# Optimization experiments

Measured on AMD Instinct MI355X. Metric: run time of the kernel, lower is better.

The kernel has to match this reference:

```python
import jax, jax.numpy as jnp
import numpy as np

MASK_INFTY_APPROX = 1e30
B, L, D = 2, 2048, 1024
H = 16
HD = D // H  # 64
NCODE = 512


def setup_inputs() -> dict:
    key = jax.random.key(0)
    ks = jax.random.split(key, 6)
    s = 1.0 / np.sqrt(D)
    x = jax.random.normal(ks[0], (B, L, D), dtype=jnp.float32)
    Wq = jax.random.normal(ks[1], (D, D), dtype=jnp.float32) * s
    Wk = jax.random.normal(ks[2], (D, D), dtype=jnp.float32) * s
    Wv = jax.random.normal(ks[3], (D, D), dtype=jnp.float32) * s
    Wo = jax.random.normal(ks[4], (D, D), dtype=jnp.float32) * s
    codebook = jax.random.normal(ks[5], (H, NCODE, HD), dtype=jnp.float32)
    return {"x": x, "Wq": Wq, "Wk": Wk, "Wv": Wv, "Wo": Wo, "codebook": codebook}


def _vq(k, codebook):
    # k: [B,H,L,hd], codebook: [H,C,hd]
    dot = jnp.einsum('bhld,hcd->bhlc', k, codebook)
    k2 = jnp.sum(k * k, axis=-1, keepdims=True)            # [B,H,L,1]
    c2 = jnp.sum(codebook * codebook, axis=-1)             # [H,C]
    d2 = k2 - 2.0 * dot + c2[None, :, None, :]             # [B,H,L,C]
    shortcodes = jnp.argmin(d2, axis=-1)                   # [B,H,L]
    h_idx = jnp.arange(H)[None, :, None]
    c_sel = codebook[h_idx, shortcodes]                    # [B,H,L,hd]
    # straight-through quantization
    k_hat = k + jax.lax.stop_gradient(c_sel - k)
    l_commit = jnp.mean(jnp.sum((k - jax.lax.stop_gradient(c_sel)) ** 2, axis=-1))
    l_codebook = jnp.mean(jnp.sum((jax.lax.stop_gradient(k) - c_sel) ** 2, axis=-1))
    return k_hat, shortcodes, l_commit, l_codebook


def reference(x, Wq, Wk, Wv, Wo, codebook):
    q = jnp.einsum('bld,de->ble', x, Wq.T).reshape(B, L, H, HD).transpose(0, 2, 1, 3)
    k = jnp.einsum('bld,de->ble', x, Wk.T).reshape(B, L, H, HD).transpose(0, 2, 1, 3)
    v = jnp.einsum('bld,de->ble', x, Wv.T).reshape(B, L, H, HD).transpose(0, 2, 1, 3)
    k_hat, shortcodes, l_commit, l_codebook = _vq(k, codebook)
    scale = HD ** (-0.5)
    logits = jnp.einsum('bhld,bhtd->bhlt', q, k_hat) * scale  # [B,H,L,L]
    causal_mask = jnp.tril(jnp.ones((L, L), dtype=bool))
    logits = jnp.where(causal_mask[None, None], logits, -MASK_INFTY_APPROX)
    w = jax.nn.softmax(logits, axis=-1)
    attn = jnp.einsum('bhlt,bhtd->bhld', w, v)
    attn = attn.transpose(0, 2, 1, 3).reshape(B, L, D)
    out = jnp.einsum('bld,de->ble', attn, Wo.T)
    return out, l_commit, l_codebook, shortcodes
```

## Files before the change

### kernel.cpp

```cpp
#include <hip/hip_runtime.h>
#include <stdint.h>

#define BB 2
#define HH 16
#define LL 2048
#define DD 1024
#define HDD 64
#define NC 512

typedef __bf16 bf16x8 __attribute__((ext_vector_type(8)));
typedef float f32x4 __attribute__((ext_vector_type(4)));
typedef unsigned short u16x8 __attribute__((ext_vector_type(8)));

__device__ __forceinline__ unsigned short f2bf(float f) {
  union { float f; unsigned u; } v; v.f = f;
  unsigned u = v.u;
  u += 0x7fffu + ((u >> 16) & 1u);
  return (unsigned short)(u >> 16);
}
__device__ __forceinline__ float bf2f(unsigned short h) {
  union { unsigned u; float f; } v; v.u = ((unsigned)h) << 16;
  return v.f;
}

__device__ __forceinline__ void load_lds16(const unsigned short* g, unsigned short* l) {
  __builtin_amdgcn_global_load_lds((const __attribute__((address_space(1))) void*)g,
                                   (__attribute__((address_space(3))) void*)l, 16, 0, 0);
}

__global__ void cast_all(const float* __restrict__ x, const float* __restrict__ wq,
                         const float* __restrict__ wk, const float* __restrict__ wv,
                         const float* __restrict__ wo, const float* __restrict__ cb,
                         unsigned short* __restrict__ xb, unsigned short* __restrict__ xl,
                         unsigned short* __restrict__ wb, unsigned short* __restrict__ wkl,
                         unsigned short* __restrict__ wob, unsigned short* __restrict__ cbb,
                         unsigned short* __restrict__ cbl, float* __restrict__ lsum) {
  long i = (long)blockIdx.x * blockDim.x + threadIdx.x;
  if (i == 0) lsum[0] = 0.f;
  const long NX = 4194304, NW = 1048576, NCB = 524288;
  const long TOT = NX + 4 * NW + NCB;
  for (long t = i; t < TOT; t += (long)gridDim.x * blockDim.x) {
    if (t < NX) {
      float v = x[t];
      unsigned short hi = f2bf(v);
      xb[t] = hi;
      xl[t] = f2bf(v - bf2f(hi));
    } else if (t < NX + NW) {
      wb[t - NX] = f2bf(wq[t - NX]);
    } else if (t < NX + 2 * NW) {
      long idx = t - NX - NW;
      float v = wk[idx];
      unsigned short hi = f2bf(v);
      wb[NW + idx] = hi;
      wkl[idx] = f2bf(v - bf2f(hi));
    } else if (t < NX + 3 * NW) {
      wb[t - NX] = f2bf(wv[t - NX - 2 * NW]);
    } else if (t < NX + 4 * NW) {
      wob[t - NX - 3 * NW] = f2bf(wo[t - NX - 3 * NW]);
    } else {
      long idx = t - NX - 4 * NW;
      float v = cb[idx];
      unsigned short hi = f2bf(v);
      cbb[idx] = hi;
      cbl[idx] = f2bf(v - bf2f(hi));
    }
  }
}

__global__ void c2_kernel(const float* __restrict__ cb, float* __restrict__ c2) {
  int i = blockIdx.x * blockDim.x + threadIdx.x;
  if (i >= HH * NC) return;
  const float* r = cb + (long)i * HDD;
  double s = 0.0;
  for (int j = 0; j < HDD; j++) s += (double)r[j] * (double)r[j];
  c2[i] = (float)s;
}

__global__ __launch_bounds__(256) void gemm_qv(
    const unsigned short* __restrict__ xb, const unsigned short* __restrict__ wb,
    unsigned short* __restrict__ qb, unsigned short* __restrict__ vt) {
  __shared__ __align__(16) unsigned short As[128 * 32];
  __shared__ __align__(16) unsigned short Bs[128 * 32];
  int tid = threadIdx.x;
  int wave = tid >> 6, lane = tid & 63;
  int quad = lane >> 4, col = lane & 15;
  int m0 = blockIdx.y * 128;
  int n0 = blockIdx.x * 128 + (blockIdx.x >= 8 ? 1024 : 0);
  f32x4 acc[4][4] = {};
  int row_in = (wave << 4) + (lane >> 2);
  int seg = lane & 3;
  const unsigned short* gA0 = xb + (long)(m0 + row_in) * DD + seg * 8;
  const unsigned short* gA1 = xb + (long)(m0 + 64 + row_in) * DD + seg * 8;
  const unsigned short* gB0 = wb + (long)(n0 + row_in) * DD + seg * 8;
  const unsigned short* gB1 = wb + (long)(n0 + 64 + row_in) * DD + seg * 8;
  unsigned short* lA0 = As + wave * 512;
  unsigned short* lA1 = As + 2048 + wave * 512;
  unsigned short* lB0 = Bs + wave * 512;
  unsigned short* lB1 = Bs + 2048 + wave * 512;
  int wm = wave & 1, wn = wave >> 1;
  const unsigned short* pa = As + (wm * 64 + col) * 32 + quad * 8;
  const unsigned short* pb = Bs + (wn * 64 + col) * 32 + quad * 8;
  for (int kk = 0; kk < DD; kk += 32) {
    __syncthreads();
    load_lds16(gA0 + kk, lA0);
    load_lds16(gA1 + kk, lA1);
    load_lds16(gB0 + kk, lB0);
    load_lds16(gB1 + kk, lB1);
    __syncthreads();
    bf16x8 af[4], bfr[4];
    for (int t = 0; t < 4; t++) af[t]  = *(const bf16x8*)(pa + t * 512);
    for (int t = 0; t < 4; t++) bfr[t] = *(const bf16x8*)(pb + t * 512);
    for (int mt = 0; mt < 4; mt++)
      for (int nt = 0; nt < 4; nt++)
        acc[mt][nt] = __builtin_amdgcn_mfma_f32_16x16x32_bf16(af[mt], bfr[nt], acc[mt][nt], 0, 0, 0);
  }
  for (int mt = 0; mt < 4; mt++)
    for (int nt = 0; nt < 4; nt++) {
      int mbase = m0 + wm * 64 + mt * 16 + quad * 4;
      int n = n0 + wn * 64 + nt * 16 + col;
      int which = n >> 10, e = n & 1023;
      int h = e >> 6, hd = e & 63;
      for (int r = 0; r < 4; r++) {
        int m = mbase + r;
        int b = m >> 11, l = m & 2047;
        unsigned short val = f2bf(acc[mt][nt][r]);
        long bh = (long)(b * HH + h);
        if (which == 0)      qb[(bh * LL + l) * HDD + hd] = val;
        else                 vt[(bh * HDD + hd) * LL + l] = val;
      }
    }
}

__global__ __launch_bounds__(256) void kgemm_split(
    const unsigned short* __restrict__ xb, const unsigned short* __restrict__ xl,
    const unsigned short* __restrict__ wb, const unsigned short* __restrict__ wkl,
    float* __restrict__ kf) {
  __shared__ __align__(16) unsigned short Ah[128 * 32];
  __shared__ __align__(16) unsigned short Al[128 * 32];
  __shared__ __align__(16) unsigned short Bh[64 * 32];
  __shared__ __align__(16) unsigned short Bl[64 * 32];
  int tid = threadIdx.x;
  int wave = tid >> 6, lane = tid & 63;
  int quad = lane >> 4, col = lane & 15;
  int n0 = blockIdx.x * 64;
  int m0 = blockIdx.y * 128;
  f32x4 acc[4][2] = {};
  int row_in = (wave << 4) + (lane >> 2);
  int seg = lane & 3;
  const unsigned short* gAh0 = xb + (long)(m0 + row_in) * DD + seg * 8;
  const unsigned short* gAh1 = xb + (long)(m0 + 64 + row_in) * DD + seg * 8;
  const unsigned short* gAl0 = xl + (long)(m0 + row_in) * DD + seg * 8;
  const unsigned short* gAl1 = xl + (long)(m0 + 64 + row_in) * DD + seg * 8;
  const unsigned short* gBh  = wb + (long)(1048576 + (long)(n0 + row_in) * DD) + seg * 8;
  const unsigned short* gBl  = wkl + (long)(n0 + row_in) * DD + seg * 8;
  unsigned short* lAh0 = Ah + wave * 512;
  unsigned short* lAh1 = Ah + 2048 + wave * 512;
  unsigned short* lAl0 = Al + wave * 512;
  unsigned short* lAl1 = Al + 2048 + wave * 512;
  unsigned short* lBh  = Bh + wave * 512;
  unsigned short* lBl  = Bl + wave * 512;
  int wm = wave & 1, wn = wave >> 1;
  const unsigned short* pah = Ah + (wm * 64 + col) * 32 + quad * 8;
  const unsigned short* pal = Al + (wm * 64 + col) * 32 + quad * 8;
  const unsigned short* pbh = Bh + (wn * 32 + col) * 32 + quad * 8;
  const unsigned short* pbl = Bl + (wn * 32 + col) * 32 + quad * 8;
  for (int kk = 0; kk < DD; kk += 32) {
    __syncthreads();
    load_lds16(gAh0 + kk, lAh0);
    load_lds16(gAh1 + kk, lAh1);
    load_lds16(gAl0 + kk, lAl0);
    load_lds16(gAl1 + kk, lAl1);
    load_lds16(gBh + kk, lBh);
    load_lds16(gBl + kk, lBl);
    __syncthreads();
    bf16x8 ah[4], al[4], bhf[2], blf[2];
    for (int t = 0; t < 4; t++) ah[t] = *(const bf16x8*)(pah + t * 512);
    for (int t = 0; t < 4; t++) al[t] = *(const bf16x8*)(pal + t * 512);
    for (int t = 0; t < 2; t++) bhf[t] = *(const bf16x8*)(pbh + t * 512);
    for (int t = 0; t < 2; t++) blf[t] = *(const bf16x8*)(pbl + t * 512);
    for (int mt = 0; mt < 4; mt++)
      for (int nt = 0; nt < 2; nt++) {
        acc[mt][nt] = __builtin_amdgcn_mfma_f32_16x16x32_bf16(ah[mt], bhf[nt], acc[mt][nt], 0, 0, 0);
        acc[mt][nt] = __builtin_amdgcn_mfma_f32_16x16x32_bf16(ah[mt], blf[nt], acc[mt][nt], 0, 0, 0);
        acc[mt][nt] = __builtin_amdgcn_mfma_f32_16x16x32_bf16(al[mt], bhf[nt], acc[mt][nt], 0, 0, 0);
      }
  }
  int h = blockIdx.x;
  for (int mt = 0; mt < 4; mt++)
    for (int nt = 0; nt < 2; nt++) {
      int mbase = m0 + wm * 64 + mt * 16 + quad * 4;
      int hd = wn * 32 + nt * 16 + col;
      for (int r = 0; r < 4; r++) {
        int m = mbase + r;
        int b = m >> 11, l = m & 2047;
        kf[((long)(b * HH + h) * LL + l) * HDD + hd] = acc[mt][nt][r];
      }
    }
}

__global__ __launch_bounds__(256) void vq_mfma(
    const float* __restrict__ kf, const float* __restrict__ cb,
    const float* __restrict__ c2, const unsigned short* __restrict__ cbb,
    const unsigned short* __restrict__ cbl,
    unsigned short* __restrict__ khat, float* __restrict__ scodes,
    float* __restrict__ lsum) {
  __shared__ __align__(16) unsigned short CbH[2][32 * 72];
  __shared__ __align__(16) unsigned short CbL[2][32 * 72];
  __shared__ int finalIdx[64];
  int tid = threadIdx.x, wave = tid >> 6, lane = tid & 63;
  int quad = lane >> 4, col = lane & 15;
  int rb = blockIdx.x;
  int bh = blockIdx.y;
  int h = bh & 15;
  int rbase = rb * 64 + wave * 16;
  const float* kp = kf + ((long)bh * LL + rbase + col) * HDD + quad * 8;
  float fv[16];
  {
    float4 t0 = *(const float4*)(kp);
    float4 t1 = *(const float4*)(kp + 4);
    float4 t2 = *(const float4*)(kp + 32);
    float4 t3 = *(const float4*)(kp + 36);
    fv[0]=t0.x; fv[1]=t0.y; fv[2]=t0.z; fv[3]=t0.w;
    fv[4]=t1.x; fv[5]=t1.y; fv[6]=t1.z; fv[7]=t1.w;
    fv[8]=t2.x; fv[9]=t2.y; fv[10]=t2.z; fv[11]=t2.w;
    fv[12]=t3.x; fv[13]=t3.y; fv[14]=t3.z; fv[15]=t3.w;
  }
  float k2 = 0.f;
#pragma unroll
  for (int j = 0; j < 16; j++) k2 = fmaf(fv[j], fv[j], k2);
  k2 += __shfl_xor(k2, 16);
  k2 += __shfl_xor(k2, 32);
  u16x8 kh0u, kh1u, kl0u, kl1u;
#pragma unroll
  for (int j = 0; j < 8; j++) {
    unsigned short hi = f2bf(fv[j]);
    kh0u[j] = hi; kl0u[j] = f2bf(fv[j] - bf2f(hi));
    unsigned short hi2 = f2bf(fv[8 + j]);
    kh1u[j] = hi2; kl1u[j] = f2bf(fv[8 + j] - bf2f(hi2));
  }
  bf16x8 bh0 = __builtin_bit_cast(bf16x8, kh0u);
  bf16x8 bh1 = __builtin_bit_cast(bf16x8, kh1u);
  bf16x8 bl0 = __builtin_bit_cast(bf16x8, kl0u);
  bf16x8 bl1 = __builtin_bit_cast(bf16x8, kl1u);
  const unsigned short* cbbh = cbb + (long)h * NC * HDD;
  const unsigned short* cblh = cbl + (long)h * NC * HDD;
  const float* c2h = c2 + h * NC;

  int srow = tid >> 3;
  int sseg = (tid & 7) * 8;
  const unsigned short* gH = cbbh + (long)srow * HDD + sseg;
  const unsigned short* gL = cblh + (long)srow * HDD + sseg;
  int ldsOff = srow * 72 + sseg;

  {
    u16x8 ph = *(const u16x8*)(gH);
    u16x8 pl = *(const u16x8*)(gL);
    *(u16x8*)(CbH[0] + ldsOff) = ph;
    *(u16x8*)(CbL[0] + ldsOff) = pl;
  }
  __syncthreads();

  float b1v = 1e38f, b2v = 1e38f;
  int b1i = 0x7fffffff, b2i = 0x7fffffff;
  for (int t = 0; t < 16; t++) {
    int cur = t & 1;
    u16x8 nh, nl;
    if (t < 15) {
      nh = *(const u16x8*)(gH + (t + 1) * 32 * HDD);
      nl = *(const u16x8*)(gL + (t + 1) * 32 * HDD);
    }
#pragma unroll
    for (int s = 0; s < 2; s++) {
      const unsigned short* rp = CbH[cur] + (s * 16 + col) * 72 + quad * 8;
      const unsigned short* rq = CbL[cur] + (s * 16 + col) * 72 + quad * 8;
      bf16x8 ah0 = *(const bf16x8*)(rp);
      bf16x8 ah1 = *(const bf16x8*)(rp + 32);
      bf16x8 al0 = *(const bf16x8*)(rq);
      bf16x8 al1 = *(const bf16x8*)(rq + 32);
      f32x4 aP = {}, aQ = {};
      aP = __builtin_amdgcn_mfma_f32_16x16x32_bf16(ah0, bh0, aP, 0, 0, 0);
      aQ = __builtin_amdgcn_mfma_f32_16x16x32_bf16(ah1, bh1, aQ, 0, 0, 0);
      aP = __builtin_amdgcn_mfma_f32_16x16x32_bf16(al0, bh0, aP, 0, 0, 0);
      aQ = __builtin_amdgcn_mfma_f32_16x16x32_bf16(al1, bh1, aQ, 0, 0, 0);
      aP = __builtin_amdgcn_mfma_f32_16x16x32_bf16(ah0, bl0, aP, 0, 0, 0);
      aQ = __builtin_amdgcn_mfma_f32_16x16x32_bf16(ah1, bl1, aQ, 0, 0, 0);
      f32x4 c2v = *(const f32x4*)(c2h + t * 32 + s * 16 + quad * 4);
#pragma unroll
      for (int r = 0; r < 4; r++) {
        float val = c2v[r] - 2.0f * (aP[r] + aQ[r]);
        int idx = t * 32 + s * 16 + quad * 4 + r;
        if (val < b1v) { b2v = b1v; b2i = b1i; b1v = val; b1i = idx; }
        else if (val < b2v) { b2v = val; b2i = idx; }
      }
    }
    if (t < 15) {
      *(u16x8*)(CbH[cur ^ 1] + ldsOff) = nh;
      *(u16x8*)(CbL[cur ^ 1] + ldsOff) = nl;
    }
    __syncthreads();
  }
#pragma unroll
  for (int d = 16; d <= 32; d <<= 1) {
    float o1v = __shfl_xor(b1v, d); int o1i = __shfl_xor(b1i, d);
    float o2v = __shfl_xor(b2v, d); int o2i = __shfl_xor(b2i, d);
    if (o1v < b1v || (o1v == b1v && o1i < b1i)) {
      float nv; int ni;
      if (b1v < o2v || (b1v == o2v && b1i < o2i)) { nv = b1v; ni = b1i; }
      else { nv = o2v; ni = o2i; }
      b1v = o1v; b1i = o1i; b2v = nv; b2i = ni;
    } else {
      if (o1v < b2v || (o1v == b2v && o1i < b2i)) { b2v = o1v; b2i = o1i; }
    }
  }
  const float DMARG = 0.015625f;
  bool trig = (b2v - b1v <= DMARG);
  float part;
  int widx = b1i;
  if (__any(trig)) {
    const float* kpr = kf + ((long)bh * LL + rbase + col) * HDD + quad * 8;
    float4 f0 = *(const float4*)(kpr);
    float4 f1 = *(const float4*)(kpr + 4);
    float4 f2 = *(const float4*)(kpr + 32);
    float4 f3 = *(const float4*)(kpr + 36);
    const float* c1p = cb + ((long)h * NC + b1i) * HDD + quad * 8;
    const float* c2p = cb + ((long)h * NC + b2i) * HDD + quad * 8;
    float4 a0 = *(const float4*)(c1p);
    float4 a1 = *(const float4*)(c1p + 4);
    float4 a2 = *(const float4*)(c1p + 32);
    float4 a3 = *(const float4*)(c1p + 36);
    float4 e0 = *(const float4*)(c2p);
    float4 e1 = *(const float4*)(c2p + 4);
    float4 e2 = *(const float4*)(c2p + 32);
    float4 e3 = *(const float4*)(c2p + 36);
    float s1 = 0.f, s2 = 0.f;
#pragma unroll
    for (int j = 0; j < 4; j++) {
      float d;
      d = ((const float*)&f0)[j] - ((const float*)&a0)[j]; s1 = fmaf(d, d, s1);
      d = ((const float*)&f1)[j] - ((const float*)&a1)[j]; s1 = fmaf(d, d, s1);
      d = ((const float*)&f2)[j] - ((const float*)&a2)[j]; s1 = fmaf(d, d, s1);
      d = ((const float*)&f3)[j] - ((const float*)&a3)[j]; s1 = fmaf(d, d, s1);
      d = ((const float*)&f0)[j] - ((const float*)&e0)[j]; s2 = fmaf(d, d, s2);
      d = ((const float*)&f1)[j] - ((const float*)&e1)[j]; s2 = fmaf(d, d, s2);
      d = ((const float*)&f2)[j] - ((const float*)&e2)[j]; s2 = fmaf(d, d, s2);
      d = ((const float*)&f3)[j] - ((const float*)&e3)[j]; s2 = fmaf(d, d, s2);
    }
    s1 += __shfl_xor(s1, 16); s1 += __shfl_xor(s1, 32);
    s2 += __shfl_xor(s2, 16); s2 += __shfl_xor(s2, 32);
    if (trig) {
      if (s2 < s1 || (s2 == s1 && b2i < b1i)) { widx = b2i; part = s2; }
      else { widx = b1i; part = s1; }
    } else {
      part = k2 + b1v;
    }
  } else {
    part = k2 + b1v;
  }
  if (quad != 0) part = 0.f;
  part += __shfl_xor(part, 1);  part += __shfl_xor(part, 2);
  part += __shfl_xor(part, 4);  part += __shfl_xor(part, 8);
  part += __shfl_xor(part, 16); part += __shfl_xor(part, 32);
  if (lane == 0) atomicAdd(lsum, part);
  if (lane < 16) {
    scodes[(long)bh * LL + rbase + lane] = (float)widx;
    finalIdx[wave * 16 + lane] = widx;
  }
  __syncthreads();
  {
    int r = tid >> 2, p = (tid & 3) * 16;
    int code = finalIdx[r];
    const unsigned short* src = cbb + ((long)h * NC + code) * HDD + p;
    unsigned short* dst = khat + ((long)bh * LL + rb * 64 + r) * HDD + p;
    *(u16x8*)(dst)     = *(const u16x8*)(src);
    *(u16x8*)(dst + 8) = *(const u16x8*)(src + 8);
  }
}

__global__ __launch_bounds__(256) void attn_kernel(
    const unsigned short* __restrict__ qb, const unsigned short* __restrict__ khat,
    const unsigned short* __restrict__ vt, unsigned short* __restrict__ attnb) {
  __shared__ __align__(16) unsigned short Pbuf[4][2][16 * 72];
  __shared__ __align__(16) unsigned short Kbuf[64 * 72];
  __shared__ __align__(16) unsigned short Vbuf[64 * 72];
  int tid = threadIdx.x, wave = tid >> 6, lane = tid & 63;
  int quad = lane >> 4, col = lane & 15;
  int pi = blockIdx.x;
  int bh = blockIdx.y;
  int b = bh >> 4, h = bh & 15;
  int ta = pi, tb = 31 - pi;
  int qbA = ta * 64 + wave * 16;
  int qbB = tb * 64 + wave * 16;
  const unsigned short* qrA = qb + ((long)bh * LL + qbA + col) * HDD;
  const unsigned short* qrB = qb + ((long)bh * LL + qbB + col) * HDD;
  bf16x8 aqA0 = *(const bf16x8*)(qrA + quad * 8);
  bf16x8 aqA1 = *(const bf16x8*)(qrA + 32 + quad * 8);
  bf16x8 aqB0 = *(const bf16x8*)(qrB + quad * 8);
  bf16x8 aqB1 = *(const bf16x8*)(qrB + 32 + quad * 8);
  float lA[4] = {0.f, 0.f, 0.f, 0.f}, lB[4] = {0.f, 0.f, 0.f, 0.f};
  f32x4 oA[4] = {}, oB[4] = {};
  unsigned short* PA = Pbuf[wave][0];
  unsigned short* PB = Pbuf[wave][1];
  const unsigned short* kh = khat + (long)bh * LL * HDD;
  const unsigned short* vh = vt + (long)bh * HDD * LL;
  int srow = tid >> 2, sc = (tid & 3) * 8;
  const unsigned short* gK = kh + (long)srow * HDD + sc;
  const unsigned short* gV = vh + (long)srow * LL + sc;
  unsigned short* lK = Kbuf + srow * 72 + sc;
  unsigned short* lV = Vbuf + srow * 72 + sc;
  const float SCL = 0.18033688011112042f;
  for (int kt = 0; kt <= tb; kt++) {
    int kbase = kt * 64;
    bool actA = (kt <= ta);
    __syncthreads();
    {
      const unsigned short* srcK = gK + (long)kbase * HDD;
      const unsigned short* srcV = gV + kbase;
      *(u16x8*)lK        = *(const u16x8*)(srcK);
      *(u16x8*)(lK + 32) = *(const u16x8*)(srcK + 32);
      *(u16x8*)lV        = *(const u16x8*)(srcV);
      *(u16x8*)(lV + 32) = *(const u16x8*)(srcV + 32);
    }
    __syncthreads();
    f32x4 zA[4], zB[4];
    for (int nt = 0; nt < 4; nt++) {
      const unsigned short* krow = Kbuf + (nt * 16 + col) * 72;
      bf16x8 k0 = *(const bf16x8*)(krow + quad * 8);
      bf16x8 k1 = *(const bf16x8*)(krow + 32 + quad * 8);
      f32x4 z = {};
      z = __builtin_amdgcn_mfma_f32_16x16x32_bf16(aqB0, k0, z, 0, 0, 0);
      z = __builtin_amdgcn_mfma_f32_16x16x32_bf16(aqB1, k1, z, 0, 0, 0);
      zB[nt] = z;
      if (actA) {
        f32x4 y = {};
        y = __builtin_amdgcn_mfma_f32_16x16x32_bf16(aqA0, k0, y, 0, 0, 0);
        y = __builtin_amdgcn_mfma_f32_16x16x32_bf16(aqA1, k1, y, 0, 0, 0);
        zA[nt] = y;
      }
    }
    for (int nt = 0; nt < 4; nt++) {
      int key = kbase + nt * 16 + col;
      for (int r = 0; r < 4; r++) {
        float sc2 = zB[nt][r] * SCL;
        if (kt == tb && key > qbB + quad * 4 + r) sc2 = -1e30f;
        float p = exp2f(sc2);
        lB[r] += p;
        PB[(quad * 4 + r) * 72 + nt * 16 + col] = __builtin_bit_cast(unsigned short, (__bf16)p);
      }
    }
    if (actA) {
      for (int nt = 0; nt < 4; nt++) {
        int key = kbase + nt * 16 + col;
        for (int r = 0; r < 4; r++) {
          float sc2 = zA[nt][r] * SCL;
          if (kt == ta && key > qbA + quad * 4 + r) sc2 = -1e30f;
          float p = exp2f(sc2);
          lA[r] += p;
          PA[(quad * 4 + r) * 72 + nt * 16 + col] = __builtin_bit_cast(unsigned short, (__bf16)p);
        }
      }
    }
    bf16x8 apB0 = *(const bf16x8*)(PB + col * 72 + quad * 8);
    bf16x8 apB1 = *(const bf16x8*)(PB + col * 72 + 32 + quad * 8);
    bf16x8 apA0, apA1;
    if (actA) {
      apA0 = *(const bf16x8*)(PA + col * 72 + quad * 8);
      apA1 = *(const bf16x8*)(PA + col * 72 + 32 + quad * 8);
    }
    for (int nt = 0; nt < 4; nt++) {
      const unsigned short* vrow = Vbuf + (nt * 16 + col) * 72;
      bf16x8 v0 = *(const bf16x8*)(vrow + quad * 8);
      bf16x8 v1 = *(const bf16x8*)(vrow + 32 + quad * 8);
      oB[nt] = __builtin_amdgcn_mfma_f32_16x16x32_bf16(apB0, v0, oB[nt], 0, 0, 0);
      oB[nt] = __builtin_amdgcn_mfma_f32_16x16x32_bf16(apB1, v1, oB[nt], 0, 0, 0);
      if (actA) {
        oA[nt] = __builtin_amdgcn_mfma_f32_16x16x32_bf16(apA0, v0, oA[nt], 0, 0, 0);
        oA[nt] = __builtin_amdgcn_mfma_f32_16x16x32_bf16(apA1, v1, oA[nt], 0, 0, 0);
      }
    }
  }
  float invA[4], invB[4];
  for (int r = 0; r < 4; r++) {
    float t = lA[r];
    t += __shfl_xor(t, 1); t += __shfl_xor(t, 2);
    t += __shfl_xor(t, 4); t += __shfl_xor(t, 8);
    invA[r] = 1.0f / t;
    float u = lB[r];
    u += __shfl_xor(u, 1); u += __shfl_xor(u, 2);
    u += __shfl_xor(u, 4); u += __shfl_xor(u, 8);
    invB[r] = 1.0f / u;
  }
  for (int r = 0; r < 4; r++) {
    int rowA = qbA + quad * 4 + r;
    int rowB = qbB + quad * 4 + r;
    for (int nt = 0; nt < 4; nt++) {
      int hd = nt * 16 + col;
      attnb[((long)b * LL + rowA) * DD + h * HDD + hd] = f2bf(oA[nt][r] * invA[r]);
      attnb[((long)b * LL + rowB) * DD + h * HDD + hd] = f2bf(oB[nt][r] * invB[r]);
    }
  }
}

__global__ __launch_bounds__(256) void gemm_out(
    const unsigned short* __restrict__ attnb, const unsigned short* __restrict__ wob,
    float* __restrict__ out) {
  __shared__ __align__(16) unsigned short As[128 * 32];
  __shared__ __align__(16) unsigned short Bs[128 * 32];
  int tid = threadIdx.x;
  int wave = tid >> 6, lane = tid & 63;
  int quad = lane >> 4, col = lane & 15;
  int m0 = blockIdx.y * 128;
  int n0 = blockIdx.x * 128;
  f32x4 acc[4][4] = {};
  int row_in = (wave << 4) + (lane >> 2);
  int seg = lane & 3;
  const unsigned short* gA0 = attnb + (long)(m0 + row_in) * DD + seg * 8;
  const unsigned short* gA1 = attnb + (long)(m0 + 64 + row_in) * DD + seg * 8;
  const unsigned short* gB0 = wob + (long)(n0 + row_in) * DD + seg * 8;
  const unsigned short* gB1 = wob + (long)(n0 + 64 + row_in) * DD + seg * 8;
  unsigned short* lA0 = As + wave * 512;
  unsigned short* lA1 = As + 2048 + wave * 512;
  unsigned short* lB0 = Bs + wave * 512;
  unsigned short* lB1 = Bs + 2048 + wave * 512;
  int wm = wave & 1, wn = wave >> 1;
  const unsigned short* pa = As + (wm * 64 + col) * 32 + quad * 8;
  const unsigned short* pb = Bs + (wn * 64 + col) * 32 + quad * 8;
  for (int kk = 0; kk < DD; kk += 32) {
    __syncthreads();
    load_lds16(gA0 + kk, lA0);
    load_lds16(gA1 + kk, lA1);
    load_lds16(gB0 + kk, lB0);
    load_lds16(gB1 + kk, lB1);
    __syncthreads();
    bf16x8 af[4], bfr[4];
    for (int t = 0; t < 4; t++) af[t]  = *(const bf16x8*)(pa + t * 512);
    for (int t = 0; t < 4; t++) bfr[t] = *(const bf16x8*)(pb + t * 512);
    for (int mt = 0; mt < 4; mt++)
      for (int nt = 0; nt < 4; nt++)
        acc[mt][nt] = __builtin_amdgcn_mfma_f32_16x16x32_bf16(af[mt], bfr[nt], acc[mt][nt], 0, 0, 0);
  }
  for (int mt = 0; mt < 4; mt++)
    for (int nt = 0; nt < 4; nt++) {
      int mbase = m0 + wm * 64 + mt * 16 + quad * 4;
      int n = n0 + wn * 64 + nt * 16 + col;
      for (int r = 0; r < 4; r++)
        out[(long)(mbase + r) * DD + n] = acc[mt][nt][r];
    }
}

__global__ void finalize(const float* __restrict__ lsum, float* __restrict__ out) {
  if (threadIdx.x == 0) {
    float v = lsum[0] / (float)(BB * HH * LL);
    out[4194304] = v;
    out[4194305] = v;
  }
}

extern "C" void kernel_launch(void* const* d_in, const int* in_sizes, int n_in,
                              void* d_out, int out_size, void* d_ws, size_t ws_size,
                              hipStream_t stream) {
  const float* x  = (const float*)d_in[0];
  const float* wq = (const float*)d_in[1];
  const float* wk = (const float*)d_in[2];
  const float* wv = (const float*)d_in[3];
  const float* wo = (const float*)d_in[4];
  const float* cb = (const float*)d_in[5];
  float* out = (float*)d_out;

  char* ws = (char*)d_ws;
  size_t off = 0;
  auto alloc = [&](size_t bytes) {
    void* p = ws + off;
    off = (off + bytes + 255) & ~(size_t)255;
    return p;
  };
  unsigned short* xb    = (unsigned short*)alloc(4194304 * 2);
  unsigned short* xl    = (unsigned short*)alloc(4194304 * 2);
  unsigned short* wb    = (unsigned short*)alloc(3145728 * 2);
  unsigned short* wkl   = (unsigned short*)alloc(1048576 * 2);
  unsigned short* wob   = (unsigned short*)alloc(1048576 * 2);
  unsigned short* cbb   = (unsigned short*)alloc(524288 * 2);
  unsigned short* cbl   = (unsigned short*)alloc(524288 * 2);
  unsigned short* qb    = (unsigned short*)alloc(4194304 * 2);
  unsigned short* vt    = (unsigned short*)alloc(4194304 * 2);
  unsigned short* khat  = (unsigned short*)alloc(4194304 * 2);
  unsigned short* attnb = (unsigned short*)alloc(4194304 * 2);
  float* kf   = (float*)alloc(4194304 * 4);
  float* c2   = (float*)alloc(8192 * 4);
  float* lsum = (float*)alloc(256);

  cast_all<<<dim3(4096), dim3(256), 0, stream>>>(x, wq, wk, wv, wo, cb, xb, xl, wb, wkl, wob, cbb, cbl, lsum);
  c2_kernel<<<dim3(32), dim3(256), 0, stream>>>(cb, c2);
  gemm_qv<<<dim3(16, 32), dim3(256), 0, stream>>>(xb, wb, qb, vt);
  kgemm_split<<<dim3(16, 32), dim3(256), 0, stream>>>(xb, xl, wb, wkl, kf);
  vq_mfma<<<dim3(32, 32), dim3(256), 0, stream>>>(kf, cb, c2, cbb, cbl, khat, out + 4194306, lsum);
  attn_kernel<<<dim3(16, 32), dim3(256), 0, stream>>>(qb, khat, vt, attnb);
  gemm_out<<<dim3(8, 32), dim3(256), 0, stream>>>(attnb, wob, out);
  finalize<<<dim3(1), dim3(64), 0, stream>>>(lsum, out);
}
```

Before: 331.9 us.

## Process two row groups per wave in VQ kernel to reuse codebook tiles

Each wave in the VQ argmin kernel now handles 32 key rows instead of 16, so every codebook tile loaded into LDS feeds twice as many MFMAs. The grid is halved to match. Codebook squared norms are staged once into shared memory rather than read from global memory each iteration. The change cuts codebook traffic and barrier count per row, at the cost of more registers and half as many blocks to spread across the GPU.

```diff
diff --git a/kernel.cpp b/kernel.cpp
--- a/kernel.cpp
+++ b/kernel.cpp
@@ -206,45 +206,53 @@
     float* __restrict__ lsum) {
   __shared__ __align__(16) unsigned short CbH[2][32 * 72];
   __shared__ __align__(16) unsigned short CbL[2][32 * 72];
-  __shared__ int finalIdx[64];
+  __shared__ __align__(16) float Cs[NC];
+  __shared__ int finalIdx[128];
   int tid = threadIdx.x, wave = tid >> 6, lane = tid & 63;
   int quad = lane >> 4, col = lane & 15;
   int rb = blockIdx.x;
   int bh = blockIdx.y;
   int h = bh & 15;
-  int rbase = rb * 64 + wave * 16;
-  const float* kp = kf + ((long)bh * LL + rbase + col) * HDD + quad * 8;
-  float fv[16];
-  {
+  int rbase = rb * 128 + wave * 32;
+  const float* c2h = c2 + h * NC;
+  Cs[tid] = c2h[tid];
+  Cs[tid + 256] = c2h[tid + 256];
+
+  bf16x8 bhf[2][2], blf[2][2];
+  float k2g[2];
+#pragma unroll
+  for (int g = 0; g < 2; g++) {
+    const float* kp = kf + ((long)bh * LL + rbase + g * 16 + col) * HDD + quad * 8;
     float4 t0 = *(const float4*)(kp);
     float4 t1 = *(const float4*)(kp + 4);
     float4 t2 = *(const float4*)(kp + 32);
     float4 t3 = *(const float4*)(kp + 36);
+    float fv[16];
     fv[0]=t0.x; fv[1]=t0.y; fv[2]=t0.z; fv[3]=t0.w;
     fv[4]=t1.x; fv[5]=t1.y; fv[6]=t1.z; fv[7]=t1.w;
     fv[8]=t2.x; fv[9]=t2.y; fv[10]=t2.z; fv[11]=t2.w;
     fv[12]=t3.x; fv[13]=t3.y; fv[14]=t3.z; fv[15]=t3.w;
-  }
-  float k2 = 0.f;
-#pragma unroll
-  for (int j = 0; j < 16; j++) k2 = fmaf(fv[j], fv[j], k2);
-  k2 += __shfl_xor(k2, 16);
-  k2 += __shfl_xor(k2, 32);
-  u16x8 kh0u, kh1u, kl0u, kl1u;
-#pragma unroll
-  for (int j = 0; j < 8; j++) {
-    unsigned short hi = f2bf(fv[j]);
-    kh0u[j] = hi; kl0u[j] = f2bf(fv[j] - bf2f(hi));
-    unsigned short hi2 = f2bf(fv[8 + j]);
-    kh1u[j] = hi2; kl1u[j] = f2bf(fv[8 + j] - bf2f(hi2));
-  }
-  bf16x8 bh0 = __builtin_bit_cast(bf16x8, kh0u);
-  bf16x8 bh1 = __builtin_bit_cast(bf16x8, kh1u);
-  bf16x8 bl0 = __builtin_bit_cast(bf16x8, kl0u);
-  bf16x8 bl1 = __builtin_bit_cast(bf16x8, kl1u);
+    float k2 = 0.f;
+#pragma unroll
+    for (int j = 0; j < 16; j++) k2 = fmaf(fv[j], fv[j], k2);
+    k2 += __shfl_xor(k2, 16);
+    k2 += __shfl_xor(k2, 32);
+    k2g[g] = k2;
+    u16x8 h0, h1, l0, l1;
+#pragma unroll
+    for (int j = 0; j < 8; j++) {
+      unsigned short hi = f2bf(fv[j]);
+      h0[j] = hi; l0[j] = f2bf(fv[j] - bf2f(hi));
+      unsigned short hi2 = f2bf(fv[8 + j]);
+      h1[j] = hi2; l1[j] = f2bf(fv[8 + j] - bf2f(hi2));
+    }
+    bhf[g][0] = __builtin_bit_cast(bf16x8, h0);
+    bhf[g][1] = __builtin_bit_cast(bf16x8, h1);
+    blf[g][0] = __builtin_bit_cast(bf16x8, l0);
+    blf[g][1] = __builtin_bit_cast(bf16x8, l1);
+  }
   const unsigned short* cbbh = cbb + (long)h * NC * HDD;
   const unsigned short* cblh = cbl + (long)h * NC * HDD;
-  const float* c2h = c2 + h * NC;
 
   int srow = tid >> 3;
   int sseg = (tid & 7) * 8;
@@ -260,8 +268,8 @@
   }
   __syncthreads();
 
-  float b1v = 1e38f, b2v = 1e38f;
-  int b1i = 0x7fffffff, b2i = 0x7fffffff;
+  float b1v[2] = {1e38f, 1e38f}, b2v[2] = {1e38f, 1e38f};
+  int b1i[2] = {0x7fffffff, 0x7fffffff}, b2i[2] = {0x7fffffff, 0x7fffffff};
   for (int t = 0; t < 16; t++) {
     int cur = t & 1;
     u16x8 nh, nl;
@@ -277,20 +285,29 @@
       bf16x8 ah1 = *(const bf16x8*)(rp + 32);
       bf16x8 al0 = *(const bf16x8*)(rq);
       bf16x8 al1 = *(const bf16x8*)(rq + 32);
-      f32x4 aP = {}, aQ = {};
-      aP = __builtin_amdgcn_mfma_f32_16x16x32_bf16(ah0, bh0, aP, 0, 0, 0);
-      aQ = __builtin_amdgcn_mfma_f32_16x16x32_bf16(ah1, bh1, aQ, 0, 0, 0);
-      aP = __builtin_amdgcn_mfma_f32_16x16x32_bf16(al0, bh0, aP, 0, 0, 0);
-      aQ = __builtin_amdgcn_mfma_f32_16x16x32_bf16(al1, bh1, aQ, 0, 0, 0);
-      aP = __builtin_amdgcn_mfma_f32_16x16x32_bf16(ah0, bl0, aP, 0, 0, 0);
-      aQ = __builtin_amdgcn_mfma_f32_16x16x32_bf16(ah1, bl1, aQ, 0, 0, 0);
-      f32x4 c2v = *(const f32x4*)(c2h + t * 32 + s * 16 + quad * 4);
+      f32x4 aP0 = {}, aQ0 = {}, aP1 = {}, aQ1 = {};
+      aP0 = __builtin_amdgcn_mfma_f32_16x16x32_bf16(ah0, bhf[0][0], aP0, 0, 0, 0);
+      aQ0 = __builtin_amdgcn_mfma_f32_16x16x32_bf16(ah1, bhf[0][1], aQ0, 0, 0, 0);
+      aP1 = __builtin_amdgcn_mfma_f32_16x16x32_bf16(ah0, bhf[1][0], aP1, 0, 0, 0);
+      aQ1 = __builtin_amdgcn_mfma_f32_16x16x32_bf16(ah1, bhf[1][1], aQ1, 0, 0, 0);
+      aP0 = __builtin_amdgcn_mfma_f32_16x16x32_bf16(al0, bhf[0][0], aP0, 0, 0, 0);
+      aQ0 = __builtin_amdgcn_mfma_f32_16x16x32_bf16(al1, bhf[0][1], aQ0, 0, 0, 0);
+      aP1 = __builtin_amdgcn_mfma_f32_16x16x32_bf16(al0, bhf[1][0], aP1, 0, 0, 0);
+      aQ1 = __builtin_amdgcn_mfma_f32_16x16x32_bf16(al1, bhf[1][1], aQ1, 0, 0, 0);
+      aP0 = __builtin_amdgcn_mfma_f32_16x16x32_bf16(ah0, blf[0][0], aP0, 0, 0, 0);
+      aQ0 = __builtin_amdgcn_mfma_f32_16x16x32_bf16(ah1, blf[0][1], aQ0, 0, 0, 0);
+      aP1 = __builtin_amdgcn_mfma_f32_16x16x32_bf16(ah0, blf[1][0], aP1, 0, 0, 0);
+      aQ1 = __builtin_amdgcn_mfma_f32_16x16x32_bf16(ah1, blf[1][1], aQ1, 0, 0, 0);
+      f32x4 c2v = *(const f32x4*)(Cs + t * 32 + s * 16 + quad * 4);
 #pragma unroll
       for (int r = 0; r < 4; r++) {
-        float val = c2v[r] - 2.0f * (aP[r] + aQ[r]);
         int idx = t * 32 + s * 16 + quad * 4 + r;
-        if (val < b1v) { b2v = b1v; b2i = b1i; b1v = val; b1i = idx; }
-        else if (val < b2v) { b2v = val; b2i = idx; }
+        float v0 = c2v[r] - 2.0f * (aP0[r] + aQ0[r]);
+        if (v0 < b1v[0]) { b2v[0] = b1v[0]; b2i[0] = b1i[0]; b1v[0] = v0; b1i[0] = idx; }
+        else if (v0 < b2v[0]) { b2v[0] = v0; b2i[0] = idx; }
+        float v1 = c2v[r] - 2.0f * (aP1[r] + aQ1[r]);
+        if (v1 < b1v[1]) { b2v[1] = b1v[1]; b2i[1] = b1i[1]; b1v[1] = v1; b1i[1] = idx; }
+        else if (v1 < b2v[1]) { b2v[1] = v1; b2i[1] = idx; }
       }
     }
     if (t < 15) {
@@ -299,80 +316,89 @@
     }
     __syncthreads();
   }
-#pragma unroll
-  for (int d = 16; d <= 32; d <<= 1) {
-    float o1v = __shfl_xor(b1v, d); int o1i = __shfl_xor(b1i, d);
-    float o2v = __shfl_xor(b2v, d); int o2i = __shfl_xor(b2i, d);
-    if (o1v < b1v || (o1v == b1v && o1i < b1i)) {
-      float nv; int ni;
-      if (b1v < o2v || (b1v == o2v && b1i < o2i)) { nv = b1v; ni = b1i; }
-      else { nv = o2v; ni = o2i; }
-      b1v = o1v; b1i = o1i; b2v = nv; b2i = ni;
+  const float DMARG = 0.015625f;
+  float partT = 0.f;
+#pragma unroll
+  for (int g = 0; g < 2; g++) {
+    float v1 = b1v[g], v2 = b2v[g];
+    int i1 = b1i[g], i2 = b2i[g];
+#pragma unroll
+    for (int d = 16; d <= 32; d <<= 1) {
+      float o1v = __shfl_xor(v1, d); int o1i = __shfl_xor(i1, d);
+      float o2v = __shfl_xor(v2, d); int o2i = __shfl_xor(i2, d);
+      if (o1v < v1 || (o1v == v1 && o1i < i1)) {
+        float nv; int ni;
+        if (v1 < o2v || (v1 == o2v && i1 < o2i)) { nv = v1; ni = i1; }
+        else { nv = o2v; ni = o2i; }
+        v1 = o1v; i1 = o1i; v2 = nv; i2 = ni;
+      } else {
+        if (o1v < v2 || (o1v == v2 && o1i < i2)) { v2 = o1v; i2 = o1i; }
+      }
+    }
+    bool trig = (v2 - v1 <= DMARG);
+    float part;
+    int widx = i1;
+    if (__any(trig)) {
+      const float* kpr = kf + ((long)bh * LL + rbase + g * 16 + col) * HDD + quad * 8;
+      float4 f0 = *(const float4*)(kpr);
+      float4 f1 = *(const float4*)(kpr + 4);
+      float4 f2 = *(const float4*)(kpr + 32);
+      float4 f3 = *(const float4*)(kpr + 36);
+      const float* c1p = cb + ((long)h * NC + i1) * HDD + quad * 8;
+      const float* c2p = cb + ((long)h * NC + i2) * HDD + quad * 8;
+      float4 a0 = *(const float4*)(c1p);
+      float4 a1 = *(const float4*)(c1p + 4);
+      float4 a2 = *(const float4*)(c1p + 32);
+      float4 a3 = *(const float4*)(c1p + 36);
+      float4 e0 = *(const float4*)(c2p);
+      float4 e1 = *(const float4*)(c2p + 4);
+      float4 e2 = *(const float4*)(c2p + 32);
+      float4 e3 = *(const float4*)(c2p + 36);
+      float s1 = 0.f, s2 = 0.f;
+#pragma unroll
+      for (int j = 0; j < 4; j++) {
+        float d;
+        d = ((const float*)&f0)[j] - ((const float*)&a0)[j]; s1 = fmaf(d, d, s1);
+        d = ((const float*)&f1)[j] - ((const float*)&a1)[j]; s1 = fmaf(d, d, s1);
+        d = ((const float*)&f2)[j] - ((const float*)&a2)[j]; s1 = fmaf(d, d, s1);
+        d = ((const float*)&f3)[j] - ((const float*)&a3)[j]; s1 = fmaf(d, d, s1);
+        d = ((const float*)&f0)[j] - ((const float*)&e0)[j]; s2 = fmaf(d, d, s2);
+        d = ((const float*)&f1)[j] - ((const float*)&e1)[j]; s2 = fmaf(d, d, s2);
+        d = ((const float*)&f2)[j] - ((const float*)&e2)[j]; s2 = fmaf(d, d, s2);
+        d = ((const float*)&f3)[j] - ((const float*)&e3)[j]; s2 = fmaf(d, d, s2);
+      }
+      s1 += __shfl_xor(s1, 16); s1 += __shfl_xor(s1, 32);
+      s2 += __shfl_xor(s2, 16); s2 += __shfl_xor(s2, 32);
+      if (trig) {
+        if (s2 < s1 || (s2 == s1 && i2 < i1)) { widx = i2; part = s2; }
+        else { widx = i1; part = s1; }
+      } else {
+        part = k2g[g] + v1;
+      }
     } else {
-      if (o1v < b2v || (o1v == b2v && o1i < b2i)) { b2v = o1v; b2i = o1i; }
-    }
-  }
-  const float DMARG = 0.015625f;
-  bool trig = (b2v - b1v <= DMARG);
-  float part;
-  int widx = b1i;
-  if (__any(trig)) {
-    const float* kpr = kf + ((long)bh * LL + rbase + col) * HDD + quad * 8;
-    float4 f0 = *(const float4*)(kpr);
-    float4 f1 = *(const float4*)(kpr + 4);
-    float4 f2 = *(const float4*)(kpr + 32);
-    float4 f3 = *(const float4*)(kpr + 36);
-    const float* c1p = cb + ((long)h * NC + b1i) * HDD + quad * 8;
-    const float* c2p = cb + ((long)h * NC + b2i) * HDD + quad * 8;
-    float4 a0 = *(const float4*)(c1p);
-    float4 a1 = *(const float4*)(c1p + 4);
-    float4 a2 = *(const float4*)(c1p + 32);
-    float4 a3 = *(const float4*)(c1p + 36);
-    float4 e0 = *(const float4*)(c2p);
-    float4 e1 = *(const float4*)(c2p + 4);
-    float4 e2 = *(const float4*)(c2p + 32);
-    float4 e3 = *(const float4*)(c2p + 36);
-    float s1 = 0.f, s2 = 0.f;
-#pragma unroll
-    for (int j = 0; j < 4; j++) {
-      float d;
-      d = ((const float*)&f0)[j] - ((const float*)&a0)[j]; s1 = fmaf(d, d, s1);
-      d = ((const float*)&f1)[j] - ((const float*)&a1)[j]; s1 = fmaf(d, d, s1);
-      d = ((const float*)&f2)[j] - ((const float*)&a2)[j]; s1 = fmaf(d, d, s1);
-      d = ((const float*)&f3)[j] - ((const float*)&a3)[j]; s1 = fmaf(d, d, s1);
-      d = ((const float*)&f0)[j] - ((const float*)&e0)[j]; s2 = fmaf(d, d, s2);
-      d = ((const float*)&f1)[j] - ((const float*)&e1)[j]; s2 = fmaf(d, d, s2);
-      d = ((const float*)&f2)[j] - ((const float*)&e2)[j]; s2 = fmaf(d, d, s2);
-      d = ((const float*)&f3)[j] - ((const float*)&e3)[j]; s2 = fmaf(d, d, s2);
-    }
-    s1 += __shfl_xor(s1, 16); s1 += __shfl_xor(s1, 32);
-    s2 += __shfl_xor(s2, 16); s2 += __shfl_xor(s2, 32);
-    if (trig) {
-      if (s2 < s1 || (s2 == s1 && b2i < b1i)) { widx = b2i; part = s2; }
-      else { widx = b1i; part = s1; }
-    } else {
-      part = k2 + b1v;
-    }
-  } else {
-    part = k2 + b1v;
-  }
-  if (quad != 0) part = 0.f;
-  part += __shfl_xor(part, 1);  part += __shfl_xor(part, 2);
-  part += __shfl_xor(part, 4);  part += __shfl_xor(part, 8);
-  part += __shfl_xor(part, 16); part += __shfl_xor(part, 32);
-  if (lane == 0) atomicAdd(lsum, part);
-  if (lane < 16) {
-    scodes[(long)bh * LL + rbase + lane] = (float)widx;
-    finalIdx[wave * 16 + lane] = widx;
-  }
+      part = k2g[g] + v1;
+    }
+    if (quad == 0) partT += part;
+    if (lane < 16) {
+      int row_local = wave * 32 + g * 16 + lane;
+      scodes[(long)bh * LL + rb * 128 + row_local] = (float)widx;
+      finalIdx[row_local] = widx;
+    }
+  }
+  partT += __shfl_xor(partT, 1);  partT += __shfl_xor(partT, 2);
+  partT += __shfl_xor(partT, 4);  partT += __shfl_xor(partT, 8);
+  partT += __shfl_xor(partT, 16); partT += __shfl_xor(partT, 32);
+  if (lane == 0) atomicAdd(lsum, partT);
   __syncthreads();
   {
-    int r = tid >> 2, p = (tid & 3) * 16;
+    int r = tid >> 1, p = (tid & 1) * 32;
     int code = finalIdx[r];
     const unsigned short* src = cbb + ((long)h * NC + code) * HDD + p;
-    unsigned short* dst = khat + ((long)bh * LL + rb * 64 + r) * HDD + p;
-    *(u16x8*)(dst)     = *(const u16x8*)(src);
-    *(u16x8*)(dst + 8) = *(const u16x8*)(src + 8);
+    unsigned short* dst = khat + ((long)bh * LL + rb * 128 + r) * HDD + p;
+    *(u16x8*)(dst)      = *(const u16x8*)(src);
+    *(u16x8*)(dst + 8)  = *(const u16x8*)(src + 8);
+    *(u16x8*)(dst + 16) = *(const u16x8*)(src + 16);
+    *(u16x8*)(dst + 24) = *(const u16x8*)(src + 24);
   }
 }
 
@@ -592,7 +618,7 @@
   c2_kernel<<<dim3(32), dim3(256), 0, stream>>>(cb, c2);
   gemm_qv<<<dim3(16, 32), dim3(256), 0, stream>>>(xb, wb, qb, vt);
   kgemm_split<<<dim3(16, 32), dim3(256), 0, stream>>>(xb, xl, wb, wkl, kf);
-  vq_mfma<<<dim3(32, 32), dim3(256), 0, stream>>>(kf, cb, c2, cbb, cbl, khat, out + 4194306, lsum);
+  vq_mfma<<<dim3(16, 32), dim3(256), 0, stream>>>(kf, cb, c2, cbb, cbl, khat, out + 4194306, lsum);
   attn_kernel<<<dim3(16, 32), dim3(256), 0, stream>>>(qb, khat, vt, attnb);
   gemm_out<<<dim3(8, 32), dim3(256), 0, stream>>>(attnb, wob, out);
   finalize<<<dim3(1), dim3(64), 0, stream>>>(lsum, out);
```

Measured after the change: 314.4 us. -5.3%, faster.
